# Performance work log

Hardware: AMD Instinct MI355X
Metric: run time of the kernel (lower is better)

Reference implementation:

```python
import jax, jax.numpy as jnp
import numpy as np

U, T, K, Q, H = 4096, 200, 64, 10000, 128
STD_THETA = 1.0


def setup_inputs() -> dict:
    key = jax.random.key(0)
    ks = jax.random.split(key, 12)
    q_id = jax.random.randint(ks[0], (U, T), 0, Q, dtype=jnp.int32)
    resp = jax.random.randint(ks[1], (U, T), 0, 2, dtype=jnp.int32)
    # one KC per question so the per-timestep masked_select size is constant (= U)
    kc_of_q = jax.random.randint(ks[2], (Q,), 0, K)
    kmap = jax.nn.one_hot(kc_of_q, K, dtype=jnp.float32) > 0.5  # (Q, K) bool, one-hot
    mask = jnp.ones((U, T), dtype=bool)
    diff_mu = jax.random.normal(ks[3], (Q,), dtype=jnp.float32)
    disc_mu = jax.random.normal(ks[4], (Q,), dtype=jnp.float32)
    xav = lambda k, fi, fo: jax.random.normal(k, (fi, fo), dtype=jnp.float32) * (2.0 / (fi + fo)) ** 0.5
    W1 = xav(ks[5], 3, H)
    W2 = xav(ks[6], H, H)
    W3 = xav(ks[7], H, 2)
    b1 = jnp.zeros((H,), jnp.float32)
    b2 = jnp.zeros((H,), jnp.float32)
    b3 = jnp.zeros((2,), jnp.float32)
    return dict(mask=mask, q_id=q_id, kmap=kmap, resp=resp,
                diff_mu=diff_mu, disc_mu=disc_mu,
                W1=W1, b1=b1, W2=W2, b2=b2, W3=W3, b3=b3)


def reference(mask, q_id, kmap, resp, diff_mu, disc_mu, W1, b1, W2, b2, W3, b3):
    gelu = lambda x: jax.nn.gelu(x, approximate=False)  # torch nn.GELU default = exact erf
    nu = q_id.shape[0]
    td = diff_mu[q_id]                      # (U, T) trial difficulty
    ts = disc_mu[q_id]                      # (U, T) trial discrimination
    x = jnp.stack([td, ts, resp.astype(jnp.float32)], axis=-1)  # (U, T, 3)
    h = gelu(gelu(x @ W1 + b1) @ W2 + b2)
    out = gelu(h @ W3 + b3)                 # (U, T, 2)
    mu = out[..., 0].T                      # (T, U)
    logvar = out[..., 1].T                  # (T, U)
    std = jnp.maximum(jnp.exp(0.5 * logvar), 1e-8)
    r = (STD_THETA / std) ** 2              # (T, U)

    # backward Kalman-style recursion: b_t = 1/(1 + r_t + (1 - b_{t+1})), c_t = b_t*(c_{t+1} + r_t*mu_t)
    def bwd_step(carry, rm):
        b_n, c_n = carry
        r_t, mu_t = rm
        b_t = 1.0 / (1.0 + r_t + (1.0 - b_n))
        c_t = b_t * (c_n + r_t * mu_t)
        return (b_t, c_t), (b_t, c_t)

    init = (jnp.ones((nu,), mu.dtype), jnp.zeros((nu,), mu.dtype))
    _, (b_seq, c_seq) = jax.lax.scan(bwd_step, init, (r, mu), reverse=True)  # (T, U) each

    # forward pass: gather active-KC ability, update, scatter back into per-user KC state
    active_kc = jnp.argmax(kmap[q_id], axis=-1).T  # (T, U) one active KC per trial
    uidx = jnp.arange(nu)

    def fwd_step(curr, bck):
        b_t, c_t, kc_t = bck
        prev = curr[uidx, kc_t]
        mu_t = b_t * prev + c_t
        curr = curr.at[uidx, kc_t].set(mu_t)
        return curr, mu_t

    curr0 = jnp.zeros((nu, kmap.shape[1]), mu.dtype)
    last_ability_kc, ability_T = jax.lax.scan(fwd_step, curr0, (b_seq, c_seq, active_kc))
    ability = ability_T.T                   # (U, T): masked mean over one-hot KC = active KC ability
    trial_logits = ts * (ability - td)      # (U, T)
    return trial_logits, last_ability_kc
```

## Files before the change

### kernel.cpp

```cpp
#include <hip/hip_runtime.h>
#include <math.h>

#define U_ 4096
#define T_ 200
#define K_ 64
#define Q_ 10000
#define H_ 128
#define UPB 8

__device__ __forceinline__ float gelu_f(float x) {
  return 0.5f * x * (1.0f + erff(x * 0.70710678118654752440f));
}

__global__ __launch_bounds__(256, 4) void mlp_table_kernel(
    const float* __restrict__ diff_mu, const float* __restrict__ disc_mu,
    const float* __restrict__ W1, const float* __restrict__ b1,
    const float* __restrict__ W2, const float* __restrict__ b2,
    const float* __restrict__ W3, const float* __restrict__ b3,
    const unsigned char* __restrict__ kmap,
    float4* __restrict__ tab4, int* __restrict__ kc_of_q) {
  __shared__ float W2s[64 * H_];
  __shared__ float h1buf[16][H_];

  const int tid = threadIdx.x;
  const int base = blockIdx.x * 16;

  for (int v = tid; v < 64 * H_; v += 256) W2s[v] = W2[v];

  if (blockIdx.x < 40) {
    int q = blockIdx.x * 256 + tid;
    if (q < Q_) {
      const unsigned char* km = kmap + (size_t)q * K_;
      int kc = 0;
#pragma unroll
      for (int k = 0; k < K_; ++k)
        if (km[k]) kc = k;
      kc_of_q[q] = kc;
    }
  }

  for (int v = tid; v < 16 * H_; v += 256) {
    int pl = v >> 7, j = v & 127;
    int pg = base + pl;
    int q = pg >> 1;
    float rf = (float)(pg & 1);
    float td = diff_mu[q], ts = disc_mu[q];
    float a = b1[j];
    a += td * W1[j];
    a += ts * W1[H_ + j];
    a += rf * W1[2 * H_ + j];
    h1buf[pl][j] = gelu_f(a);
  }
  __syncthreads();

  const int w = tid >> 6, lane = tid & 63;
  float a0[4] = {0.f, 0.f, 0.f, 0.f}, a1[4] = {0.f, 0.f, 0.f, 0.f};
  const float* h1w = &h1buf[w * 4][0];

#pragma clang loop unroll_count(8)
  for (int k = 0; k < 64; ++k) {
    float w0 = W2s[k * H_ + lane];
    float w1 = W2s[k * H_ + lane + 64];
#pragma unroll
    for (int p = 0; p < 4; ++p) {
      float hv = h1w[p * H_ + k];
      a0[p] = fmaf(w0, hv, a0[p]);
      a1[p] = fmaf(w1, hv, a1[p]);
    }
  }
  __syncthreads();
  for (int v = tid; v < 64 * H_; v += 256) W2s[v] = W2[64 * H_ + v];
  __syncthreads();
#pragma clang loop unroll_count(8)
  for (int k = 0; k < 64; ++k) {
    float w0 = W2s[k * H_ + lane];
    float w1 = W2s[k * H_ + lane + 64];
#pragma unroll
    for (int p = 0; p < 4; ++p) {
      float hv = h1w[p * H_ + 64 + k];
      a0[p] = fmaf(w0, hv, a0[p]);
      a1[p] = fmaf(w1, hv, a1[p]);
    }
  }

  float w30a = W3[lane * 2 + 0], w31a = W3[lane * 2 + 1];
  float w30b = W3[(lane + 64) * 2 + 0], w31b = W3[(lane + 64) * 2 + 1];
  float b2a = b2[lane], b2b = b2[lane + 64];
  float b30 = b3[0], b31 = b3[1];
#pragma unroll
  for (int p = 0; p < 4; ++p) {
    float h2a = gelu_f(a0[p] + b2a);
    float h2b = gelu_f(a1[p] + b2b);
    float s0 = h2a * w30a + h2b * w30b;
    float s1 = h2a * w31a + h2b * w31b;
#pragma unroll
    for (int off = 32; off > 0; off >>= 1) {
      s0 += __shfl_xor(s0, off, 64);
      s1 += __shfl_xor(s1, off, 64);
    }
    if (lane == 0) {
      float mu = gelu_f(s0 + b30);
      float lv = gelu_f(s1 + b31);
      float sd = fmaxf(expf(0.5f * lv), 1e-8f);
      int pg = base + w * 4 + p;
      int q = pg >> 1;
      tab4[pg] = make_float4(1.0f / (sd * sd), mu, disc_mu[q], diff_mu[q]);
    }
  }
}

__global__ __launch_bounds__(512) void scan2_kernel(
    const int* __restrict__ q_id, const int* __restrict__ resp,
    const float4* __restrict__ tab4, const int* __restrict__ kc_of_q,
    float* __restrict__ out) {
  __shared__ float2 bcs[T_ * (UPB + 1)];
  __shared__ unsigned char kcs[T_ * UPB];

  const int tid = threadIdx.x;
  const int lane = tid & 63;
  const int ul = tid >> 6;
  const int gu = blockIdx.x * UPB + ul;

  float tts[4], ttd[4];
  const int* qrow = q_id + (size_t)gu * T_;
  const int* rrow = resp + (size_t)gu * T_;
#pragma unroll
  for (int tile = 0; tile < 4; ++tile) {
    int t = tile * 64 + lane;
    if (t < T_) {
      int q = qrow[t];
      int rp = rrow[t];
      float4 f = tab4[q * 2 + rp];
      bcs[t * (UPB + 1) + ul] = make_float2(f.x, f.y);
      kcs[t * UPB + ul] = (unsigned char)kc_of_q[q];
      tts[tile] = f.z;
      ttd[tile] = f.w;
    }
  }
  __syncthreads();

  if (tid < 64) {
    const bool act = lane < UPB;
    const int ll = act ? lane : 0;
    float b = 1.0f, c = 0.0f;
#pragma unroll 8
    for (int t = T_ - 1; t >= 0; --t) {
      float2 rm_ = bcs[t * (UPB + 1) + ll];
      float x_ = 2.0f + rm_.x - b;
      float ib = __builtin_amdgcn_rcpf(x_);
      ib = ib * (2.0f - x_ * ib);
      b = ib;
      c = b * fmaf(rm_.x, rm_.y, c);
      if (act) bcs[t * (UPB + 1) + lane] = make_float2(b, c);
    }
  }
  __syncthreads();

  float x = 0.0f;
#pragma unroll 8
  for (int t = 0; t < T_; ++t) {
    float2 bc_ = bcs[t * (UPB + 1) + ul];
    int kc = (int)kcs[t * UPB + ul];
    float xn = fmaf(bc_.x, x, bc_.y);
    bool hit = (lane == kc);
    x = hit ? xn : x;
    if (hit) bcs[t * (UPB + 1) + ul].x = xn;
  }
  __syncthreads();

  float* logits = out;
  float* last = out + (size_t)U_ * T_;
#pragma unroll
  for (int tile = 0; tile < 4; ++tile) {
    int t = tile * 64 + lane;
    if (t < T_) {
      float ab = bcs[t * (UPB + 1) + ul].x;
      logits[(size_t)gu * T_ + t] = tts[tile] * (ab - ttd[tile]);
    }
  }
  last[(size_t)gu * K_ + lane] = x;
}

extern "C" void kernel_launch(void* const* d_in, const int* in_sizes, int n_in,
                              void* d_out, int out_size, void* d_ws,
                              size_t ws_size, hipStream_t stream) {
  const int* q_id = (const int*)d_in[1];
  const unsigned char* kmap = (const unsigned char*)d_in[2];
  const int* resp = (const int*)d_in[3];
  const float* diff_mu = (const float*)d_in[4];
  const float* disc_mu = (const float*)d_in[5];
  const float* W1 = (const float*)d_in[6];
  const float* b1 = (const float*)d_in[7];
  const float* W2 = (const float*)d_in[8];
  const float* b2 = (const float*)d_in[9];
  const float* W3 = (const float*)d_in[10];
  const float* b3 = (const float*)d_in[11];
  float* out = (float*)d_out;
  char* ws = (char*)d_ws;

  auto align512 = [](size_t x) { return (x + 511) & ~(size_t)511; };
  size_t o = 0;
  float4* tab4 = (float4*)(ws + o);  o = align512(o + (size_t)2 * Q_ * 16);
  int* kc_of_q = (int*)(ws + o);     o = align512(o + (size_t)Q_ * 4);
  (void)ws_size; (void)in_sizes; (void)n_in; (void)out_size;

  mlp_table_kernel<<<1250, 256, 0, stream>>>(diff_mu, disc_mu, W1, b1, W2, b2,
                                             W3, b3, kmap, tab4, kc_of_q);
  scan2_kernel<<<U_ / UPB, 512, 0, stream>>>(q_id, resp, tab4, kc_of_q, out);
}
```

Measured before the change: 137.0 us.

## Double MLP pairs per block and make the backward scan per-wavefront without barriers

The MLP table kernel now handles 32 (question, response) pairs per block instead of 16. W2 is staged into shared memory with float4 copies, so each shared-memory load of W2 is reused across twice as many rows, at the cost of more accumulator registers. In the scan kernel, each wavefront now runs the backward Kalman recursion for its own user, with all lanes redundant and each lane capturing the (b, c) values for its own timesteps. This removes the single-wave serial phase and the block-wide __syncthreads barriers. The per-user serial recursion length stays the same, and every wave now spends ALU work on the redundant backward pass.

```diff
diff --git a/kernel.cpp b/kernel.cpp
--- a/kernel.cpp
+++ b/kernel.cpp
@@ -7,6 +7,7 @@
 #define Q_ 10000
 #define H_ 128
 #define UPB 8
+#define PPB 32
 
 __device__ __forceinline__ float gelu_f(float x) {
   return 0.5f * x * (1.0f + erff(x * 0.70710678118654752440f));
@@ -20,12 +21,11 @@
     const unsigned char* __restrict__ kmap,
     float4* __restrict__ tab4, int* __restrict__ kc_of_q) {
   __shared__ float W2s[64 * H_];
-  __shared__ float h1buf[16][H_];
+  __shared__ float h1buf[PPB][H_ + 1];
 
   const int tid = threadIdx.x;
-  const int base = blockIdx.x * 16;
-
-  for (int v = tid; v < 64 * H_; v += 256) W2s[v] = W2[v];
+  const int lane = tid & 63, w = tid >> 6;
+  const int base = blockIdx.x * PPB;
 
   if (blockIdx.x < 40) {
     int q = blockIdx.x * 256 + tid;
@@ -39,45 +39,45 @@
     }
   }
 
-  for (int v = tid; v < 16 * H_; v += 256) {
+  for (int v = tid; v < PPB * H_; v += 256) {
     int pl = v >> 7, j = v & 127;
-    int pg = base + pl;
-    int q = pg >> 1;
+    int pg = base + pl, q = pg >> 1;
     float rf = (float)(pg & 1);
-    float td = diff_mu[q], ts = disc_mu[q];
-    float a = b1[j];
-    a += td * W1[j];
-    a += ts * W1[H_ + j];
-    a += rf * W1[2 * H_ + j];
+    float a = fmaf(diff_mu[q], W1[j], b1[j]);
+    a = fmaf(disc_mu[q], W1[H_ + j], a);
+    a = fmaf(rf, W1[2 * H_ + j], a);
     h1buf[pl][j] = gelu_f(a);
   }
+  for (int v = tid; v < 2048; v += 256)
+    ((float4*)W2s)[v] = ((const float4*)W2)[v];
   __syncthreads();
 
-  const int w = tid >> 6, lane = tid & 63;
-  float a0[4] = {0.f, 0.f, 0.f, 0.f}, a1[4] = {0.f, 0.f, 0.f, 0.f};
-  const float* h1w = &h1buf[w * 4][0];
-
-#pragma clang loop unroll_count(8)
+  float a0[8], a1[8];
+#pragma unroll
+  for (int p = 0; p < 8; ++p) { a0[p] = 0.f; a1[p] = 0.f; }
+
+#pragma clang loop unroll_count(4)
   for (int k = 0; k < 64; ++k) {
     float w0 = W2s[k * H_ + lane];
     float w1 = W2s[k * H_ + lane + 64];
 #pragma unroll
-    for (int p = 0; p < 4; ++p) {
-      float hv = h1w[p * H_ + k];
+    for (int p = 0; p < 8; ++p) {
+      float hv = h1buf[w * 8 + p][k];
       a0[p] = fmaf(w0, hv, a0[p]);
       a1[p] = fmaf(w1, hv, a1[p]);
     }
   }
   __syncthreads();
-  for (int v = tid; v < 64 * H_; v += 256) W2s[v] = W2[64 * H_ + v];
+  for (int v = tid; v < 2048; v += 256)
+    ((float4*)W2s)[v] = ((const float4*)W2)[2048 + v];
   __syncthreads();
-#pragma clang loop unroll_count(8)
+#pragma clang loop unroll_count(4)
   for (int k = 0; k < 64; ++k) {
     float w0 = W2s[k * H_ + lane];
     float w1 = W2s[k * H_ + lane + 64];
 #pragma unroll
-    for (int p = 0; p < 4; ++p) {
-      float hv = h1w[p * H_ + 64 + k];
+    for (int p = 0; p < 8; ++p) {
+      float hv = h1buf[w * 8 + p][64 + k];
       a0[p] = fmaf(w0, hv, a0[p]);
       a1[p] = fmaf(w1, hv, a1[p]);
     }
@@ -88,7 +88,7 @@
   float b2a = b2[lane], b2b = b2[lane + 64];
   float b30 = b3[0], b31 = b3[1];
 #pragma unroll
-  for (int p = 0; p < 4; ++p) {
+  for (int p = 0; p < 8; ++p) {
     float h2a = gelu_f(a0[p] + b2a);
     float h2b = gelu_f(a1[p] + b2b);
     float s0 = h2a * w30a + h2b * w30b;
@@ -102,14 +102,14 @@
       float mu = gelu_f(s0 + b30);
       float lv = gelu_f(s1 + b31);
       float sd = fmaxf(expf(0.5f * lv), 1e-8f);
-      int pg = base + w * 4 + p;
+      int pg = base + w * 8 + p;
       int q = pg >> 1;
       tab4[pg] = make_float4(1.0f / (sd * sd), mu, disc_mu[q], diff_mu[q]);
     }
   }
 }
 
-__global__ __launch_bounds__(512) void scan2_kernel(
+__global__ __launch_bounds__(512) void scan_kernel(
     const int* __restrict__ q_id, const int* __restrict__ resp,
     const float4* __restrict__ tab4, const int* __restrict__ kc_of_q,
     float* __restrict__ out) {
@@ -125,36 +125,56 @@
   const int* qrow = q_id + (size_t)gu * T_;
   const int* rrow = resp + (size_t)gu * T_;
 #pragma unroll
-  for (int tile = 0; tile < 4; ++tile) {
-    int t = tile * 64 + lane;
+  for (int i = 0; i < 4; ++i) {
+    int t = i * 64 + lane;
+    int tc = t < T_ ? t : T_ - 1;
+    int q = qrow[tc];
+    int rp = rrow[tc];
+    float4 f = tab4[q * 2 + rp];
+    tts[i] = f.z;
+    ttd[i] = f.w;
     if (t < T_) {
-      int q = qrow[t];
-      int rp = rrow[t];
-      float4 f = tab4[q * 2 + rp];
       bcs[t * (UPB + 1) + ul] = make_float2(f.x, f.y);
       kcs[t * UPB + ul] = (unsigned char)kc_of_q[q];
-      tts[tile] = f.z;
-      ttd[tile] = f.w;
-    }
-  }
-  __syncthreads();
-
-  if (tid < 64) {
-    const bool act = lane < UPB;
-    const int ll = act ? lane : 0;
-    float b = 1.0f, c = 0.0f;
+    }
+  }
+
+  float tb[4], tcc[4];
+  float b = 1.0f, c = 0.0f;
 #pragma unroll 8
-    for (int t = T_ - 1; t >= 0; --t) {
-      float2 rm_ = bcs[t * (UPB + 1) + ll];
-      float x_ = 2.0f + rm_.x - b;
+  for (int s = 7; s >= 0; --s) {
+    int t = 192 + s;
+    float2 rm = bcs[t * (UPB + 1) + ul];
+    float x_ = 2.0f + rm.x - b;
+    float ib = __builtin_amdgcn_rcpf(x_);
+    ib = ib * (2.0f - x_ * ib);
+    b = ib;
+    c = b * fmaf(rm.x, rm.y, c);
+    bool cap = (lane == s);
+    tb[3] = cap ? b : tb[3];
+    tcc[3] = cap ? c : tcc[3];
+  }
+#pragma unroll
+  for (int i = 2; i >= 0; --i) {
+#pragma unroll 8
+    for (int s = 63; s >= 0; --s) {
+      int t = i * 64 + s;
+      float2 rm = bcs[t * (UPB + 1) + ul];
+      float x_ = 2.0f + rm.x - b;
       float ib = __builtin_amdgcn_rcpf(x_);
       ib = ib * (2.0f - x_ * ib);
       b = ib;
-      c = b * fmaf(rm_.x, rm_.y, c);
-      if (act) bcs[t * (UPB + 1) + lane] = make_float2(b, c);
-    }
-  }
-  __syncthreads();
+      c = b * fmaf(rm.x, rm.y, c);
+      bool cap = (lane == s);
+      tb[i] = cap ? b : tb[i];
+      tcc[i] = cap ? c : tcc[i];
+    }
+  }
+#pragma unroll
+  for (int i = 0; i < 4; ++i) {
+    int t = i * 64 + lane;
+    if (t < T_) bcs[t * (UPB + 1) + ul] = make_float2(tb[i], tcc[i]);
+  }
 
   float x = 0.0f;
 #pragma unroll 8
@@ -166,16 +186,15 @@
     x = hit ? xn : x;
     if (hit) bcs[t * (UPB + 1) + ul].x = xn;
   }
-  __syncthreads();
 
   float* logits = out;
   float* last = out + (size_t)U_ * T_;
 #pragma unroll
-  for (int tile = 0; tile < 4; ++tile) {
-    int t = tile * 64 + lane;
+  for (int i = 0; i < 4; ++i) {
+    int t = i * 64 + lane;
     if (t < T_) {
       float ab = bcs[t * (UPB + 1) + ul].x;
-      logits[(size_t)gu * T_ + t] = tts[tile] * (ab - ttd[tile]);
+      logits[(size_t)gu * T_ + t] = tts[i] * (ab - ttd[i]);
     }
   }
   last[(size_t)gu * K_ + lane] = x;
@@ -204,7 +223,7 @@
   int* kc_of_q = (int*)(ws + o);     o = align512(o + (size_t)Q_ * 4);
   (void)ws_size; (void)in_sizes; (void)n_in; (void)out_size;
 
-  mlp_table_kernel<<<1250, 256, 0, stream>>>(diff_mu, disc_mu, W1, b1, W2, b2,
-                                             W3, b3, kmap, tab4, kc_of_q);
-  scan2_kernel<<<U_ / UPB, 512, 0, stream>>>(q_id, resp, tab4, kc_of_q, out);
-}
+  mlp_table_kernel<<<Q_ * 2 / PPB, 256, 0, stream>>>(
+      diff_mu, disc_mu, W1, b1, W2, b2, W3, b3, kmap, tab4, kc_of_q);
+  scan_kernel<<<U_ / UPB, 512, 0, stream>>>(q_id, resp, tab4, kc_of_q, out);
+}
```

Measured after the change: 138.8 us. About the same (+1.3%).
